# Kernel tuning notes

Measured on AMD Instinct MI355X. Metric: run time of the kernel, lower is better.

Reference implementation:

```python
import jax, jax.numpy as jnp
import numpy as np

B, S, D, H = 4, 2048, 512, 8
DK = D // H


def setup_inputs() -> dict:
    key = jax.random.key(0)
    ks = jax.random.split(key, 11)
    scale = 1.0 / np.sqrt(D)
    inp = {
        'q': jax.random.normal(ks[0], (B, S, D), jnp.float32),
        'k': jax.random.normal(ks[1], (B, S, D), jnp.float32),
        'v': jax.random.normal(ks[2], (B, S, D), jnp.float32),
        'mask': jnp.tril(jnp.ones((S, S), jnp.int32))[None, None, :, :],  # [1,1,S,S] causal
        'w_q': jax.random.normal(ks[3], (D, D), jnp.float32) * scale,
        'b_q': jnp.zeros((D,), jnp.float32),
        'w_k': jax.random.normal(ks[4], (D, D), jnp.float32) * scale,
        'b_k': jnp.zeros((D,), jnp.float32),
        'w_v': jax.random.normal(ks[5], (D, D), jnp.float32) * scale,
        'b_v': jnp.zeros((D,), jnp.float32),
        'w_o': jax.random.normal(ks[6], (D, D), jnp.float32) * scale,
        'b_o': jnp.zeros((D,), jnp.float32),
    }
    return inp


def reference(q, k, v, mask, w_q, b_q, w_k, b_k, w_v, b_v, w_o, b_o):
    # QKV projections (nn.Linear: x @ W^T + b)
    def split_heads(x):  # [B,S,D] -> [B,H,S,DK]
        return x.reshape(B, S, H, DK).transpose(0, 2, 1, 3)

    qh = split_heads(q @ w_q.T + b_q)
    kh = split_heads(k @ w_k.T + b_k)
    vh = split_heads(v @ w_v.T + b_v)

    scores = jnp.einsum('bhqd,bhkd->bhqk', qh, kh) / jnp.sqrt(jnp.float32(DK))
    scores = jnp.where(mask == 0, jnp.float32(-1e9), scores)
    attn = jax.nn.softmax(scores, axis=-1)  # dropout is identity in eval
    ctx = jnp.einsum('bhqk,bhkd->bhqd', attn, vh)  # [B,H,S,DK]
    ctx = ctx.transpose(0, 2, 1, 3).reshape(B, S, D)
    return ctx @ w_o.T + b_o
```

## Files before the change

### kernel.cpp

```cpp
#include <hip/hip_runtime.h>
#include <hip/hip_bf16.h>


#define BATCH  4
#define SLEN   2048
#define DMODEL 512
#define NHEAD  8
#define DHEAD  64
#define MROWS  (BATCH * SLEN)

#define NQ ((size_t)MROWS * DMODEL)
#define NW ((size_t)DMODEL * DMODEL)
#define NB ((size_t)DMODEL)
#define CVTW_TOTAL (4 * NW + 4 * NB)

#define SCALE_L2E 0.180336880f

typedef short bf16x8 __attribute__((ext_vector_type(8)));
typedef float f32x4  __attribute__((ext_vector_type(4)));

typedef unsigned int __attribute__((address_space(1))) glb_u32_t;
typedef unsigned int __attribute__((address_space(3))) lds_u32_t;

__device__ __forceinline__ void async16(const void* g, void* l) {
    __builtin_amdgcn_global_load_lds((glb_u32_t*)g, (lds_u32_t*)l, 16, 0, 0);
}

__device__ __forceinline__ float bf2f(unsigned short u) {
    union { unsigned int i; float f; } v; v.i = ((unsigned int)u) << 16; return v.f;
}
__device__ __forceinline__ unsigned short f2bf(float f) {
    union { float f; unsigned int i; } v; v.f = f;
    unsigned int x = v.i;
    return (unsigned short)((x + 0x7fffu + ((x >> 16) & 1u)) >> 16);
}
__device__ __forceinline__ unsigned int pkbf(float a, float b) {
    union { __hip_bfloat162 h; unsigned int u; } cv;
    cv.h = __float22bfloat162_rn(float2{a, b});
    return cv.u;
}

__device__ __forceinline__ void wait0_barrier() {
    asm volatile("s_waitcnt vmcnt(0)" ::: "memory");
    __builtin_amdgcn_s_barrier();
    asm volatile("" ::: "memory");
}

__global__ __launch_bounds__(256)
void cvt_w_kernel(const float* __restrict__ wq, const float* __restrict__ wk,
                  const float* __restrict__ wv, const float* __restrict__ wo,
                  const float* __restrict__ bq, const float* __restrict__ bk,
                  const float* __restrict__ bv, const float* __restrict__ bo,
                  unsigned short* __restrict__ dst)
{
    const size_t i4 = ((size_t)blockIdx.x * 256 + threadIdx.x) * 4;
    if (i4 >= CVTW_TOTAL) return;
    const float* src;
    size_t off;
    if      (i4 <     NW)          { src = wq; off = i4; }
    else if (i4 < 2 * NW)          { src = wk; off = i4 - NW; }
    else if (i4 < 3 * NW)          { src = wv; off = i4 - 2 * NW; }
    else if (i4 < 4 * NW)          { src = wo; off = i4 - 3 * NW; }
    else if (i4 < 4 * NW + NB)     { src = bq; off = i4 - 4 * NW; }
    else if (i4 < 4 * NW + 2 * NB) { src = bk; off = i4 - 4 * NW - NB; }
    else if (i4 < 4 * NW + 3 * NB) { src = bv; off = i4 - 4 * NW - 2 * NB; }
    else                           { src = bo; off = i4 - 4 * NW - 3 * NB; }
    const float4 f = *(const float4*)(src + off);
    ushort4 o;
    o.x = f2bf(f.x); o.y = f2bf(f.y); o.z = f2bf(f.z); o.w = f2bf(f.w);
    *(ushort4*)(dst + i4) = o;
}

__device__ __forceinline__ void qkv_body(const float* __restrict__ A,
                                         const unsigned short* __restrict__ W,
                                         const unsigned short* __restrict__ bias,
                                         unsigned short* __restrict__ C,
                                         int mode, int m0, int n0,
                                         unsigned char* smem)
{
    float*          Asf = (float*)smem;
    unsigned short* Bs  = (unsigned short*)(smem + 32768);

    const int tid  = threadIdx.x;
    const int wave = tid >> 6;
    const int lane = tid & 63;
    const int l15  = lane & 15;
    const int quad = lane >> 4;
    const int wm   = (wave & 1) * 64;
    const int wn   = (wave >> 1) * 64;
    const int srow = lane >> 2;
    const int scol = (((lane & 3) ^ (srow & 3)) * 8);
    const int rswb = (quad ^ (l15 & 3)) * 8;
    const int krow = lane >> 3;
    const int acol = ((lane & 7) ^ (krow & 7)) * 4;

    auto stageA = [&](int k0, int buf) {
        #pragma unroll
        for (int c = 0; c < 4; c++) {
            const int rb = c * 32 + wave * 8;
            async16(A + (size_t)(m0 + rb + krow) * DMODEL + k0 + acol,
                    Asf + (size_t)buf * 4096 + rb * 32);
        }
    };
    auto stageW = [&](int k0, int buf) {
        async16(W + (size_t)(n0 + wave * 16 + srow) * DMODEL + k0 + scol,
                Bs + (size_t)buf * 4096 + wave * 512);
        async16(W + (size_t)(n0 + (wave + 4) * 16 + srow) * DMODEL + k0 + scol,
                Bs + (size_t)buf * 4096 + (wave + 4) * 512);
    };

    f32x4 acc[4][4] = {};
    stageA(0, 0);
    stageW(0, 0);

    #pragma unroll 1
    for (int kt = 0; kt < 16; kt++) {
        const int cur = kt & 1;
        wait0_barrier();
        if (kt < 15) { stageA((kt + 1) * 32, cur ^ 1); stageW((kt + 1) * 32, cur ^ 1); }

        bf16x8 af[4], bfr[4];
        #pragma unroll
        for (int i = 0; i < 4; i++) {
            const int row = wm + i * 16 + l15;
            const float* rp = Asf + (size_t)cur * 4096 + row * 32;
            const f32x4 x = *(const f32x4*)(rp + (((quad * 2)     ^ (row & 7)) * 4));
            const f32x4 y = *(const f32x4*)(rp + (((quad * 2 + 1) ^ (row & 7)) * 4));
            union { bf16x8 v; unsigned int u[4]; } r;
            r.u[0] = pkbf(x[0], x[1]); r.u[1] = pkbf(x[2], x[3]);
            r.u[2] = pkbf(y[0], y[1]); r.u[3] = pkbf(y[2], y[3]);
            af[i] = r.v;
        }
        #pragma unroll
        for (int j = 0; j < 4; j++)
            bfr[j] = *(const bf16x8*)(Bs + (size_t)cur * 4096 + (wn + j * 16 + l15) * 32 + rswb);
        #pragma unroll
        for (int i = 0; i < 4; i++)
            #pragma unroll
            for (int j = 0; j < 4; j++)
                acc[i][j] = __builtin_amdgcn_mfma_f32_16x16x32_bf16(af[i], bfr[j], acc[i][j], 0, 0, 0);
    }

    if (mode == 2) {
        #pragma unroll
        for (int j = 0; j < 4; j++) {
            const int col = n0 + wn + j * 16 + l15;
            const float bv = bf2f(bias[col]);
            const int hh = col >> 6, dk = col & 63;
            #pragma unroll
            for (int i = 0; i < 4; i++) {
                const int row = m0 + wm + i * 16 + quad * 4;
                const int bb = row >> 11, s = row & 2047;
                uint2 o2;
                o2.x = pkbf(acc[i][j][0] + bv, acc[i][j][1] + bv);
                o2.y = pkbf(acc[i][j][2] + bv, acc[i][j][3] + bv);
                *(uint2*)(C + ((size_t)((bb * NHEAD + hh) * DHEAD + dk)) * SLEN + s) = o2;
            }
        }
    } else {
        const float oscale = (mode == 0) ? SCALE_L2E : 1.0f;
        #pragma unroll
        for (int j = 0; j < 4; j++) {
            const int col = n0 + wn + j * 16 + l15;
            const float bv = bf2f(bias[col]);
            #pragma unroll
            for (int i = 0; i < 4; i++) {
                const int row = m0 + wm + i * 16 + quad * 4;
                #pragma unroll
                for (int r = 0; r < 4; r++)
                    C[(size_t)(row + r) * DMODEL + col] = f2bf((acc[i][j][r] + bv) * oscale);
            }
        }
    }
}

__global__ __launch_bounds__(256, 3)
void qkv_gemm_kernel(const float* __restrict__ qin, const float* __restrict__ kin,
                     const float* __restrict__ vin,
                     const unsigned short* __restrict__ wq, const unsigned short* __restrict__ bq,
                     const unsigned short* __restrict__ wk, const unsigned short* __restrict__ bk,
                     const unsigned short* __restrict__ wv, const unsigned short* __restrict__ bv,
                     unsigned short* __restrict__ qh, unsigned short* __restrict__ kh,
                     unsigned short* __restrict__ vt)
{
    __shared__ __align__(16) unsigned char smem[49152];
    const int z = blockIdx.z;
    const float*          A    = (z == 0) ? qin : (z == 1) ? kin : vin;
    const unsigned short* W    = (z == 0) ? wq  : (z == 1) ? wk  : wv;
    const unsigned short* bias = (z == 0) ? bq  : (z == 1) ? bk  : bv;
    unsigned short*       C    = (z == 0) ? qh  : (z == 1) ? kh  : vt;
    qkv_body(A, W, bias, C, z, blockIdx.x * 128, blockIdx.y * 128, smem);
}

__global__ __launch_bounds__(256, 4)
void attn_kernel(const unsigned short* __restrict__ qh,
                 const unsigned short* __restrict__ kh,
                 const unsigned short* __restrict__ vt,
                 unsigned short* __restrict__ ctx)
{
    __shared__ __align__(16) unsigned short Ks[2][64 * 64];
    __shared__ __align__(16) unsigned short Vs[2][64 * 64];
    __shared__ __align__(16) unsigned short Ps[4][16 * 64];

    const int tid  = threadIdx.x;
    const int wave = tid >> 6;
    const int lane = tid & 63;
    const int l15  = lane & 15;
    const int quad = lane >> 4;

    const int bh = blockIdx.x;
    const int x  = blockIdx.y;
    const int g  = x & 7, s = x >> 3;
    const int qt = (s == 0) ? g : (s == 1) ? 15 - g : (s == 2) ? 16 + g : 31 - g;
    const int b  = bh >> 3;
    const int h  = bh & 7;

    const size_t base = (size_t)b * SLEN * DMODEL + (size_t)h * DHEAD;
    const unsigned short* Q  = qh + base;
    const unsigned short* K  = kh + base;
    const unsigned short* VT = vt + (size_t)bh * DHEAD * SLEN;

    const int krow_l = lane >> 3;
    const int kcol_l = ((lane & 7) ^ (krow_l & 7)) * 8;

    const int qrow = qt * 64 + wave * 16 + l15;
    const bf16x8 qf0 = *(const bf16x8*)(Q + (size_t)qrow * DMODEL + quad * 8);
    const bf16x8 qf1 = *(const bf16x8*)(Q + (size_t)qrow * DMODEL + 32 + quad * 8);

    int kf_off[2][4];
    int pf_off[2];
    int pw_off[4];
    #pragma unroll
    for (int kk = 0; kk < 2; kk++) {
        pf_off[kk] = l15 * 64 + (((kk * 4 + quad) ^ (l15 & 7)) * 8);
        #pragma unroll
        for (int j = 0; j < 4; j++)
            kf_off[kk][j] = (j * 16 + l15) * 64 + (((kk * 4 + quad) ^ (l15 & 7)) * 8);
    }
    #pragma unroll
    for (int j = 0; j < 4; j++)
        pw_off[j] = l15 * 64 + (((j * 2 + (quad >> 1)) ^ (l15 & 7)) * 8) + (quad & 1) * 4;

    f32x4 oacc[4] = {};
    float lsum = 0.0f;
    unsigned short* Pw = &Ps[wave][0];
    const int ktiles = qt + 1;

    auto stageKV = [&](int kt, int buf) {
        async16(K + (size_t)(kt * 64 + wave * 8 + krow_l) * DMODEL + kcol_l,
                &Ks[buf][0] + wave * 512);
        async16(K + (size_t)(kt * 64 + (wave + 4) * 8 + krow_l) * DMODEL + kcol_l,
                &Ks[buf][0] + (wave + 4) * 512);
        async16(VT + (size_t)(wave * 8 + krow_l) * SLEN + kt * 64 + kcol_l,
                &Vs[buf][0] + wave * 512);
        async16(VT + (size_t)((wave + 4) * 8 + krow_l) * SLEN + kt * 64 + kcol_l,
                &Vs[buf][0] + (wave + 4) * 512);
    };

    auto iterbody = [&](int kt, int cur) {
        wait0_barrier();
        if (kt + 1 < ktiles) stageKV(kt + 1, cur ^ 1);

        f32x4 sacc[4] = {};
        __builtin_amdgcn_s_setprio(1);
        #pragma unroll
        for (int kk = 0; kk < 2; kk++) {
            const bf16x8 qf = kk ? qf1 : qf0;
            #pragma unroll
            for (int j = 0; j < 4; j++) {
                bf16x8 kf = *(const bf16x8*)(&Ks[cur][0] + kf_off[kk][j]);
                sacc[j] = __builtin_amdgcn_mfma_f32_16x16x32_bf16(kf, qf, sacc[j], 0, 0, 0);
            }
        }
        __builtin_amdgcn_s_setprio(0);

        if (kt == qt) {
            #pragma unroll
            for (int j = 0; j < 4; j++)
                #pragma unroll
                for (int r = 0; r < 4; r++) {
                    const int kv = kt * 64 + j * 16 + quad * 4 + r;
                    if (kv > qrow) sacc[j][r] = -1e30f;
                }
        }

        #pragma unroll
        for (int j = 0; j < 4; j++) {
            const float p0 = exp2f(sacc[j][0]);
            const float p1 = exp2f(sacc[j][1]);
            const float p2v = exp2f(sacc[j][2]);
            const float p3 = exp2f(sacc[j][3]);
            lsum += (p0 + p1) + (p2v + p3);
            uint2 pw;
            pw.x = pkbf(p0, p1);
            pw.y = pkbf(p2v, p3);
            *(uint2*)(Pw + pw_off[j]) = pw;
        }
        asm volatile("s_waitcnt lgkmcnt(0)" ::: "memory");

        __builtin_amdgcn_s_setprio(1);
        #pragma unroll
        for (int kk = 0; kk < 2; kk++) {
            bf16x8 pf = *(const bf16x8*)(Pw + pf_off[kk]);
            #pragma unroll
            for (int jd = 0; jd < 4; jd++) {
                bf16x8 vf = *(const bf16x8*)(&Vs[cur][0] + kf_off[kk][jd]);
                oacc[jd] = __builtin_amdgcn_mfma_f32_16x16x32_bf16(vf, pf, oacc[jd], 0, 0, 0);
            }
        }
        __builtin_amdgcn_s_setprio(0);
    };

    stageKV(0, 0);

    #pragma unroll 1
    for (int kt = 0; kt < ktiles; kt += 2) {
        iterbody(kt, 0);
        if (kt + 1 < ktiles) iterbody(kt + 1, 1);
    }

    lsum += __shfl_xor(lsum, 16, 64);
    lsum += __shfl_xor(lsum, 32, 64);
    const float invl = 1.0f / lsum;

    #pragma unroll
    for (int jd = 0; jd < 4; jd++) {
        uint2 o2;
        o2.x = pkbf(oacc[jd][0] * invl, oacc[jd][1] * invl);
        o2.y = pkbf(oacc[jd][2] * invl, oacc[jd][3] * invl);
        *(uint2*)(ctx + base + (size_t)qrow * DMODEL + jd * 16 + quad * 4) = o2;
    }
}

__device__ __forceinline__ void oproj_body(const unsigned short* __restrict__ ctx,
                                           const unsigned short* __restrict__ wo,
                                           const unsigned short* __restrict__ bo,
                                           float* __restrict__ out,
                                           int m0, int n0, unsigned char* smem)
{
    unsigned short* As = (unsigned short*)smem;
    unsigned short* Bs = As + 2 * 64 * 32;

    const int tid  = threadIdx.x;
    const int wave = tid >> 6;
    const int lane = tid & 63;
    const int l15  = lane & 15;
    const int quad = lane >> 4;
    const int wm   = (wave & 1) * 32;
    const int wn   = (wave >> 1) * 32;
    const int srow = lane >> 2;
    const int scol = (((lane & 3) ^ (srow & 3)) * 8);
    const int rsw  = (quad ^ (l15 & 3)) * 8;

    auto stage = [&](int k0, int buf) {
        async16(ctx + (size_t)(m0 + wave * 16 + srow) * DMODEL + k0 + scol,
                As + (size_t)buf * 2048 + wave * 512);
        async16(wo + (size_t)(n0 + wave * 16 + srow) * DMODEL + k0 + scol,
                Bs + (size_t)buf * 2048 + wave * 512);
    };

    f32x4 acc[2][2] = {};
    stage(0, 0);

    #pragma unroll 1
    for (int kt = 0; kt < 16; kt++) {
        const int cur = kt & 1;
        wait0_barrier();
        if (kt < 15) stage((kt + 1) * 32, cur ^ 1);

        bf16x8 af[2], bfr[2];
        #pragma unroll
        for (int i = 0; i < 2; i++)
            af[i] = *(const bf16x8*)(As + (size_t)cur * 2048 + (wm + i * 16 + l15) * 32 + rsw);
        #pragma unroll
        for (int j = 0; j < 2; j++)
            bfr[j] = *(const bf16x8*)(Bs + (size_t)cur * 2048 + (wn + j * 16 + l15) * 32 + rsw);
        #pragma unroll
        for (int i = 0; i < 2; i++)
            #pragma unroll
            for (int j = 0; j < 2; j++)
                acc[i][j] = __builtin_amdgcn_mfma_f32_16x16x32_bf16(af[i], bfr[j], acc[i][j], 0, 0, 0);
    }

    #pragma unroll
    for (int j = 0; j < 2; j++) {
        const int col = n0 + wn + j * 16 + l15;
        const float bv = bf2f(bo[col]);
        #pragma unroll
        for (int i = 0; i < 2; i++) {
            const int row = m0 + wm + i * 16 + quad * 4;
            #pragma unroll
            for (int r = 0; r < 4; r++)
                out[(size_t)(row + r) * DMODEL + col] = acc[i][j][r] + bv;
        }
    }
}

__global__ __launch_bounds__(256, 4)
void oproj_gemm_kernel(const unsigned short* __restrict__ ctx,
                       const unsigned short* __restrict__ wo,
                       const unsigned short* __restrict__ bo,
                       float* __restrict__ out)
{
    __shared__ __align__(16) unsigned char smem[16384];
    oproj_body(ctx, wo, bo, out, blockIdx.x * 64, blockIdx.y * 64, smem);
}

extern "C" void kernel_launch(void* const* d_in, const int* in_sizes, int n_in,
                              void* d_out, int out_size, void* d_ws, size_t ws_size,
                              hipStream_t stream)
{
    const float* q   = (const float*)d_in[0];
    const float* k   = (const float*)d_in[1];
    const float* v   = (const float*)d_in[2];
    const float* w_q = (const float*)d_in[4];
    const float* b_q = (const float*)d_in[5];
    const float* w_k = (const float*)d_in[6];
    const float* b_k = (const float*)d_in[7];
    const float* w_v = (const float*)d_in[8];
    const float* b_v = (const float*)d_in[9];
    const float* w_o = (const float*)d_in[10];
    const float* b_o = (const float*)d_in[11];
    float* out = (float*)d_out;
    unsigned short* ws = (unsigned short*)d_ws;

    unsigned short* wqb = ws + 3 * NQ;
    unsigned short* wkb = wqb + NW;
    unsigned short* wvb = wkb + NW;
    unsigned short* wob = wvb + NW;
    unsigned short* bqb = wob + NW;
    unsigned short* bkb = bqb + NB;
    unsigned short* bvb = bkb + NB;
    unsigned short* bob = bvb + NB;
    unsigned short* qh  = bob + NB;
    unsigned short* kh  = qh + NQ;
    unsigned short* vt  = kh + NQ;
    unsigned short* ctx = vt + NQ;

    dim3 blk(256);
    hipLaunchKernelGGL(cvt_w_kernel, dim3((unsigned)(CVTW_TOTAL / 4 / 256)), blk, 0, stream,
                       w_q, w_k, w_v, w_o, b_q, b_k, b_v, b_o, wqb);
    hipLaunchKernelGGL(qkv_gemm_kernel, dim3(MROWS / 128, DMODEL / 128, 3), blk, 0, stream,
                       q, k, v, wqb, bqb, wkb, bkb, wvb, bvb, qh, kh, vt);
    hipLaunchKernelGGL(attn_kernel, dim3(BATCH * NHEAD, 32), blk, 0, stream,
                       qh, kh, vt, ctx);
    hipLaunchKernelGGL(oproj_gemm_kernel, dim3(MROWS / 64, DMODEL / 64), blk, 0, stream,
                       ctx, wob, bob, out);
}
```

Measured before the change: 197.6 us.

## Process two 16-row query sub-tiles per wave in attention with 128-thread blocks

The attention kernel now uses 2 waves per block instead of 4, and each wave handles 32 query rows as two 16-row sub-tiles. Each K and V fragment read from LDS feeds two MFMAs, halving LDS traffic per unit of compute. The K/V staging loop is rewritten so the two waves still load full 64x64 tiles, and the two-iteration unrolled loop becomes a single loop. The cost is doubled accumulator registers per wave and fewer waves per block to hide latency; the occupancy hint changes from (256,4) to (128,2).

Measured after the change: 210.5 us. 1.07x slower.

```diff
diff --git a/kernel.cpp b/kernel.cpp
--- a/kernel.cpp
+++ b/kernel.cpp
@@ -192,7 +192,7 @@
     qkv_body(A, W, bias, C, z, blockIdx.x * 128, blockIdx.y * 128, smem);
 }
 
-__global__ __launch_bounds__(256, 4)
+__global__ __launch_bounds__(128, 2)
 void attn_kernel(const unsigned short* __restrict__ qh,
                  const unsigned short* __restrict__ kh,
                  const unsigned short* __restrict__ vt,
@@ -200,7 +200,7 @@
 {
     __shared__ __align__(16) unsigned short Ks[2][64 * 64];
     __shared__ __align__(16) unsigned short Vs[2][64 * 64];
-    __shared__ __align__(16) unsigned short Ps[4][16 * 64];
+    __shared__ __align__(16) unsigned short Ps[2][2][16 * 64];
 
     const int tid  = threadIdx.x;
     const int wave = tid >> 6;
@@ -223,9 +223,12 @@
     const int krow_l = lane >> 3;
     const int kcol_l = ((lane & 7) ^ (krow_l & 7)) * 8;
 
-    const int qrow = qt * 64 + wave * 16 + l15;
-    const bf16x8 qf0 = *(const bf16x8*)(Q + (size_t)qrow * DMODEL + quad * 8);
-    const bf16x8 qf1 = *(const bf16x8*)(Q + (size_t)qrow * DMODEL + 32 + quad * 8);
+    const int qrowA = qt * 64 + wave * 32 + l15;
+    const int qrowB = qrowA + 16;
+    const bf16x8 qa0 = *(const bf16x8*)(Q + (size_t)qrowA * DMODEL + quad * 8);
+    const bf16x8 qa1 = *(const bf16x8*)(Q + (size_t)qrowA * DMODEL + 32 + quad * 8);
+    const bf16x8 qb0 = *(const bf16x8*)(Q + (size_t)qrowB * DMODEL + quad * 8);
+    const bf16x8 qb1 = *(const bf16x8*)(Q + (size_t)qrowB * DMODEL + 32 + quad * 8);
 
     int kf_off[2][4];
     int pf_off[2];
@@ -241,49 +244,24 @@
     for (int j = 0; j < 4; j++)
         pw_off[j] = l15 * 64 + (((j * 2 + (quad >> 1)) ^ (l15 & 7)) * 8) + (quad & 1) * 4;
 
-    f32x4 oacc[4] = {};
-    float lsum = 0.0f;
-    unsigned short* Pw = &Ps[wave][0];
+    f32x4 oaccA[4] = {}, oaccB[4] = {};
+    float lsumA = 0.0f, lsumB = 0.0f;
+    unsigned short* PwA = &Ps[wave][0][0];
+    unsigned short* PwB = &Ps[wave][1][0];
     const int ktiles = qt + 1;
 
     auto stageKV = [&](int kt, int buf) {
-        async16(K + (size_t)(kt * 64 + wave * 8 + krow_l) * DMODEL + kcol_l,
-                &Ks[buf][0] + wave * 512);
-        async16(K + (size_t)(kt * 64 + (wave + 4) * 8 + krow_l) * DMODEL + kcol_l,
-                &Ks[buf][0] + (wave + 4) * 512);
-        async16(VT + (size_t)(wave * 8 + krow_l) * SLEN + kt * 64 + kcol_l,
-                &Vs[buf][0] + wave * 512);
-        async16(VT + (size_t)((wave + 4) * 8 + krow_l) * SLEN + kt * 64 + kcol_l,
-                &Vs[buf][0] + (wave + 4) * 512);
+        #pragma unroll
+        for (int c = 0; c < 4; c++) {
+            const int rb = wave * 32 + c * 8;
+            async16(K + (size_t)(kt * 64 + rb + krow_l) * DMODEL + kcol_l,
+                    &Ks[buf][0] + (wave * 4 + c) * 512);
+            async16(VT + (size_t)(rb + krow_l) * SLEN + kt * 64 + kcol_l,
+                    &Vs[buf][0] + (wave * 4 + c) * 512);
+        }
     };
 
-    auto iterbody = [&](int kt, int cur) {
-        wait0_barrier();
-        if (kt + 1 < ktiles) stageKV(kt + 1, cur ^ 1);
-
-        f32x4 sacc[4] = {};
-        __builtin_amdgcn_s_setprio(1);
-        #pragma unroll
-        for (int kk = 0; kk < 2; kk++) {
-            const bf16x8 qf = kk ? qf1 : qf0;
-            #pragma unroll
-            for (int j = 0; j < 4; j++) {
-                bf16x8 kf = *(const bf16x8*)(&Ks[cur][0] + kf_off[kk][j]);
-                sacc[j] = __builtin_amdgcn_mfma_f32_16x16x32_bf16(kf, qf, sacc[j], 0, 0, 0);
-            }
-        }
-        __builtin_amdgcn_s_setprio(0);
-
-        if (kt == qt) {
-            #pragma unroll
-            for (int j = 0; j < 4; j++)
-                #pragma unroll
-                for (int r = 0; r < 4; r++) {
-                    const int kv = kt * 64 + j * 16 + quad * 4 + r;
-                    if (kv > qrow) sacc[j][r] = -1e30f;
-                }
-        }
-
+    auto packP = [&](f32x4* sacc, unsigned short* Pw, float& lsum) {
         #pragma unroll
         for (int j = 0; j < 4; j++) {
             const float p0 = exp2f(sacc[j][0]);
@@ -296,39 +274,86 @@
             pw.y = pkbf(p2v, p3);
             *(uint2*)(Pw + pw_off[j]) = pw;
         }
+    };
+
+    stageKV(0, 0);
+
+    #pragma unroll 1
+    for (int kt = 0; kt < ktiles; kt++) {
+        const int cur = kt & 1;
+        wait0_barrier();
+        if (kt + 1 < ktiles) stageKV(kt + 1, cur ^ 1);
+
+        f32x4 sa[4] = {}, sb[4] = {};
+        __builtin_amdgcn_s_setprio(1);
+        #pragma unroll
+        for (int kk = 0; kk < 2; kk++) {
+            const bf16x8 qA = kk ? qa1 : qa0;
+            const bf16x8 qB = kk ? qb1 : qb0;
+            #pragma unroll
+            for (int j = 0; j < 4; j++) {
+                bf16x8 kf = *(const bf16x8*)(&Ks[cur][0] + kf_off[kk][j]);
+                sa[j] = __builtin_amdgcn_mfma_f32_16x16x32_bf16(kf, qA, sa[j], 0, 0, 0);
+                sb[j] = __builtin_amdgcn_mfma_f32_16x16x32_bf16(kf, qB, sb[j], 0, 0, 0);
+            }
+        }
+        __builtin_amdgcn_s_setprio(0);
+
+        if (kt == qt) {
+            #pragma unroll
+            for (int j = 0; j < 4; j++)
+                #pragma unroll
+                for (int r = 0; r < 4; r++) {
+                    const int kv = kt * 64 + j * 16 + quad * 4 + r;
+                    if (kv > qrowA) sa[j][r] = -1e30f;
+                    if (kv > qrowB) sb[j][r] = -1e30f;
+                }
+        }
+
+        packP(sa, PwA, lsumA);
+        packP(sb, PwB, lsumB);
         asm volatile("s_waitcnt lgkmcnt(0)" ::: "memory");
 
         __builtin_amdgcn_s_setprio(1);
         #pragma unroll
         for (int kk = 0; kk < 2; kk++) {
-            bf16x8 pf = *(const bf16x8*)(Pw + pf_off[kk]);
+            bf16x8 pfA = *(const bf16x8*)(PwA + pf_off[kk]);
+            bf16x8 pfB = *(const bf16x8*)(PwB + pf_off[kk]);
             #pragma unroll
             for (int jd = 0; jd < 4; jd++) {
                 bf16x8 vf = *(const bf16x8*)(&Vs[cur][0] + kf_off[kk][jd]);
-                oacc[jd] = __builtin_amdgcn_mfma_f32_16x16x32_bf16(vf, pf, oacc[jd], 0, 0, 0);
+                oaccA[jd] = __builtin_amdgcn_mfma_f32_16x16x32_bf16(vf, pfA, oaccA[jd], 0, 0, 0);
+                oaccB[jd] = __builtin_amdgcn_mfma_f32_16x16x32_bf16(vf, pfB, oaccB[jd], 0, 0, 0);
             }
         }
         __builtin_amdgcn_s_setprio(0);
-    };
-
-    stageKV(0, 0);
-
-    #pragma unroll 1
-    for (int kt = 0; kt < ktiles; kt += 2) {
-        iterbody(kt, 0);
-        if (kt + 1 < ktiles) iterbody(kt + 1, 1);
-    }
-
-    lsum += __shfl_xor(lsum, 16, 64);
-    lsum += __shfl_xor(lsum, 32, 64);
-    const float invl = 1.0f / lsum;
-
-    #pragma unroll
-    for (int jd = 0; jd < 4; jd++) {
-        uint2 o2;
-        o2.x = pkbf(oacc[jd][0] * invl, oacc[jd][1] * invl);
-        o2.y = pkbf(oacc[jd][2] * invl, oacc[jd][3] * invl);
-        *(uint2*)(ctx + base + (size_t)qrow * DMODEL + jd * 16 + quad * 4) = o2;
+    }
+
+    {
+        float la = lsumA;
+        la += __shfl_xor(la, 16, 64);
+        la += __shfl_xor(la, 32, 64);
+        const float invl = 1.0f / la;
+        #pragma unroll
+        for (int jd = 0; jd < 4; jd++) {
+            uint2 o2;
+            o2.x = pkbf(oaccA[jd][0] * invl, oaccA[jd][1] * invl);
+            o2.y = pkbf(oaccA[jd][2] * invl, oaccA[jd][3] * invl);
+            *(uint2*)(ctx + base + (size_t)qrowA * DMODEL + jd * 16 + quad * 4) = o2;
+        }
+    }
+    {
+        float lb = lsumB;
+        lb += __shfl_xor(lb, 16, 64);
+        lb += __shfl_xor(lb, 32, 64);
+        const float invl = 1.0f / lb;
+        #pragma unroll
+        for (int jd = 0; jd < 4; jd++) {
+            uint2 o2;
+            o2.x = pkbf(oaccB[jd][0] * invl, oaccB[jd][1] * invl);
+            o2.y = pkbf(oaccB[jd][2] * invl, oaccB[jd][3] * invl);
+            *(uint2*)(ctx + base + (size_t)qrowB * DMODEL + jd * 16 + quad * 4) = o2;
+        }
     }
 }
 
@@ -442,7 +467,7 @@
                        w_q, w_k, w_v, w_o, b_q, b_k, b_v, b_o, wqb);
     hipLaunchKernelGGL(qkv_gemm_kernel, dim3(MROWS / 128, DMODEL / 128, 3), blk, 0, stream,
                        q, k, v, wqb, bqb, wkb, bkb, wvb, bvb, qh, kh, vt);
-    hipLaunchKernelGGL(attn_kernel, dim3(BATCH * NHEAD, 32), blk, 0, stream,
+    hipLaunchKernelGGL(attn_kernel, dim3(BATCH * NHEAD, 32), dim3(128), 0, stream,
                        qh, kh, vt, ctx);
     hipLaunchKernelGGL(oproj_gemm_kernel, dim3(MROWS / 64, DMODEL / 64), blk, 0, stream,
                        ctx, wob, bob, out);
```
